# Kernel tuning notes

Measured on AMD Instinct MI355X. Metric: run time of the kernel, lower is better.

The kernel has to match this reference:

```python
import jax, jax.numpy as jnp
import numpy as np

B, H, W, DIM, WS, NH, HID = 16, 64, 64, 256, 8, 8, 1024
SHIFT = WS // 2
N = WS * WS  # tokens per window


def _rel_pos_index(ws):
    coords = np.stack(np.meshgrid(np.arange(ws), np.arange(ws), indexing='ij')).reshape(2, -1)
    rel = (coords[:, :, None] - coords[:, None, :]).transpose(1, 2, 0)  # [n,n,2]
    rel[..., 0] += ws - 1
    rel[..., 1] += ws - 1
    rel[..., 0] *= 2 * ws - 1
    return rel.sum(-1)  # [n,n] ints in [0, (2ws-1)^2)


def _attn_mask(h, w, ws, ss):
    img = np.zeros((h, w), np.float32)
    cnt = 0
    sl = (slice(0, -ws), slice(-ws, -ss), slice(-ss, None))
    for hs in sl:
        for wsl in sl:
            img[hs, wsl] = cnt
            cnt += 1
    mw = img.reshape(h // ws, ws, w // ws, ws).transpose(0, 2, 1, 3).reshape(-1, ws * ws)
    d = mw[:, None, :] - mw[:, :, None]  # unsqueeze(1) - unsqueeze(2)
    return np.where(d != 0, np.float32(-100.0), np.float32(0.0))  # [nW,n,n]


RPI = jnp.asarray(_rel_pos_index(WS).reshape(-1))          # [n*n] int
MASK = jnp.asarray(_attn_mask(H, W, WS, SHIFT))            # [nW,n,n]


def ln(x, g, b, eps):
    m = x.mean(-1, keepdims=True)
    v = x.var(-1, keepdims=True)
    return (x - m) / jnp.sqrt(v + eps) * g + b


def win_part(x, ws):
    b, h, w, c = x.shape
    x = x.reshape(b, h // ws, ws, w // ws, ws, c).transpose(0, 1, 3, 2, 4, 5)
    return x.reshape(-1, ws * ws, c)  # [b*nW, n, c]


def win_rev(win, ws, h, w):
    c = win.shape[-1]
    b = win.shape[0] // ((h // ws) * (w // ws))
    x = win.reshape(b, h // ws, w // ws, ws, ws, c).transpose(0, 1, 3, 2, 4, 5)
    return x.reshape(b, h, w, c)


def attention(xw, qkv_w, qkv_b, rpb, out_w, out_b, mask):
    Bw, n, c = xw.shape
    dh = c // NH
    scale = dh ** -0.5
    qkv = (xw @ qkv_w + qkv_b).reshape(Bw, n, 3, NH, dh).transpose(2, 0, 3, 1, 4)
    q, k, v = qkv[0], qkv[1], qkv[2]                       # [Bw,NH,n,dh]
    dots = jnp.einsum('bhid,bhjd->bhij', q, k) * scale
    bias = rpb[RPI].reshape(n, n, NH).transpose(2, 0, 1)   # [NH,n,n]
    attn = dots + bias[None]
    if mask is not None:
        nW = mask.shape[0]
        attn = attn.reshape(Bw // nW, nW, NH, n, n) + mask[None, :, None]
        attn = attn.reshape(Bw, NH, n, n)
    attn = jax.nn.softmax(attn, axis=-1)
    out = jnp.einsum('bhij,bhjd->bhid', attn, v)
    out = out.transpose(0, 2, 1, 3).reshape(Bw, n, c)
    return out @ out_w + out_b


def block(x, shifted, mask, n1g, n1b, qkv_w, qkv_b, rpb, out_w, out_b,
          n2g, n2b, lng, lnb, w1, b1, w2, b2):
    b, l, c = x.shape
    shortcut = x
    x = ln(x, n1g, n1b, 1e-5).reshape(b, H, W, c)
    if shifted:
        x = jnp.roll(x, (-SHIFT, -SHIFT), (1, 2))
    xw = win_part(x, WS)
    xw = attention(xw, qkv_w, qkv_b, rpb, out_w, out_b, mask)
    x = win_rev(xw, WS, H, W)
    if shifted:
        x = jnp.roll(x, (SHIFT, SHIFT), (1, 2))
    x = shortcut + x.reshape(b, l, c)
    # FeedForward contains its own LayerNorm(eps=1e-6) after norm2 (faithful to source)
    h = ln(x, n2g, n2b, 1e-5)
    h = ln(h, lng, lnb, 1e-6)
    h = jax.nn.gelu(h @ w1 + b1, approximate=False) @ w2 + b2
    return x + h


def forward(x, *p):
    x = block(x, False, None, *p[0:15])
    x = block(x, True, MASK, *p[15:30])
    return x


def setup_inputs() -> dict:
    key = jax.random.key(0)
    ks = iter(jax.random.split(key, 16))
    s = 0.02
    d = {'x': jax.random.normal(next(ks), (B, H * W, DIM), jnp.float32)}
    for i in (0, 1):
        p = f'b{i}_'
        d[p + 'n1g'] = jnp.ones((DIM,), jnp.float32)
        d[p + 'n1b'] = jnp.zeros((DIM,), jnp.float32)
        d[p + 'qkv_w'] = jax.random.normal(next(ks), (DIM, 3 * DIM), jnp.float32) * s
        d[p + 'qkv_b'] = jnp.zeros((3 * DIM,), jnp.float32)
        d[p + 'rpb'] = jax.random.normal(next(ks), ((2 * WS - 1) ** 2, NH), jnp.float32) * s
        d[p + 'out_w'] = jax.random.normal(next(ks), (DIM, DIM), jnp.float32) * s
        d[p + 'out_b'] = jnp.zeros((DIM,), jnp.float32)
        d[p + 'n2g'] = jnp.ones((DIM,), jnp.float32)
        d[p + 'n2b'] = jnp.zeros((DIM,), jnp.float32)
        d[p + 'lng'] = jnp.ones((DIM,), jnp.float32)
        d[p + 'lnb'] = jnp.zeros((DIM,), jnp.float32)
        d[p + 'w1'] = jax.random.normal(next(ks), (DIM, HID), jnp.float32) * s
        d[p + 'b1'] = jnp.zeros((HID,), jnp.float32)
        d[p + 'w2'] = jax.random.normal(next(ks), (HID, DIM), jnp.float32) * s
        d[p + 'b2'] = jnp.zeros((DIM,), jnp.float32)
    return d


def reference(x,
              b0_n1g, b0_n1b, b0_qkv_w, b0_qkv_b, b0_rpb, b0_out_w, b0_out_b,
              b0_n2g, b0_n2b, b0_lng, b0_lnb, b0_w1, b0_b1, b0_w2, b0_b2,
              b1_n1g, b1_n1b, b1_qkv_w, b1_qkv_b, b1_rpb, b1_out_w, b1_out_b,
              b1_n2g, b1_n2b, b1_lng, b1_lnb, b1_w1, b1_b1, b1_w2, b1_b2):
    return forward(x,
                   b0_n1g, b0_n1b, b0_qkv_w, b0_qkv_b, b0_rpb, b0_out_w, b0_out_b,
                   b0_n2g, b0_n2b, b0_lng, b0_lnb, b0_w1, b0_b1, b0_w2, b0_b2,
                   b1_n1g, b1_n1b, b1_qkv_w, b1_qkv_b, b1_rpb, b1_out_w, b1_out_b,
                   b1_n2g, b1_n2b, b1_lng, b1_lnb, b1_w1, b1_b1, b1_w2, b1_b2)
```

## Files before the change

### kernel.cpp

```cpp
#include <hip/hip_runtime.h>

typedef unsigned short u16;
typedef __attribute__((ext_vector_type(8))) short bf16x8;
typedef __attribute__((ext_vector_type(8))) unsigned short u16x8;
typedef __attribute__((ext_vector_type(4))) unsigned short u16x4;
typedef __attribute__((ext_vector_type(4))) float f32x4;

__device__ inline float b2f(u16 u) {
    union { unsigned u32; float f; } x; x.u32 = ((unsigned)u) << 16; return x.f;
}
__device__ inline u16 f2b(float f) {
    union { float f; unsigned u; } x; x.f = f;
    unsigned r = x.u + 0x7fffu + ((x.u >> 16) & 1u);
    return (u16)(r >> 16);
}

__device__ inline float fast_gelu(float v) {
    float x = fabsf(v) * 0.70710678118654752f;
    float t = __builtin_amdgcn_rcpf(1.0f + 0.3275911f * x);
    float e = __expf(-x * x);
    float poly = ((((1.061405429f * t - 1.453152027f) * t + 1.421413741f) * t
                   - 0.284496736f) * t + 0.254829592f) * t;
    float erfv = 1.0f - poly * e;
    float w = copysignf(erfv, v);
    return 0.5f * v * (1.0f + w);
}

#define GLOAD_LDS16(g, l) \
    __builtin_amdgcn_global_load_lds((const __attribute__((address_space(1))) void*)(const void*)(g), \
                                     (__attribute__((address_space(3))) void*)(void*)(l), 16, 0, 0)
#define FENCE() asm volatile("" ::: "memory")

__global__ __launch_bounds__(256)
void ln_win_kernel(const float* __restrict__ x, const float* __restrict__ g,
                   const float* __restrict__ b, u16* __restrict__ xw, int shift)
{
    int wid = blockIdx.x * 4 + (threadIdx.x >> 6);
    int lane = threadIdx.x & 63;
    int win = wid >> 6, tok = wid & 63;
    int bb = win >> 6, wib = win & 63;
    int h = (((wib >> 3) << 3) + (tok >> 3) + shift) & 63;
    int w = (((wib & 7) << 3) + (tok & 7) + shift) & 63;
    size_t src = ((size_t)bb * 4096 + h * 64 + w) * 256;
    float4 v = ((const float4*)(x + src))[lane];
    float s = v.x + v.y + v.z + v.w;
    float s2 = v.x*v.x + v.y*v.y + v.z*v.z + v.w*v.w;
    for (int k = 32; k > 0; k >>= 1) { s += __shfl_xor(s, k); s2 += __shfl_xor(s2, k); }
    float mean = s * (1.f/256.f);
    float var  = s2 * (1.f/256.f) - mean*mean;
    float rs = rsqrtf(var + 1e-5f);
    int c = lane * 4;
    u16x4 o;
    o[0] = f2b((v.x - mean) * rs * g[c+0] + b[c+0]);
    o[1] = f2b((v.y - mean) * rs * g[c+1] + b[c+1]);
    o[2] = f2b((v.z - mean) * rs * g[c+2] + b[c+2]);
    o[3] = f2b((v.w - mean) * rs * g[c+3] + b[c+3]);
    *(u16x4*)(xw + (size_t)wid * 256 + c) = o;
}

__global__ __launch_bounds__(256)
void ln2_kernel(const float* __restrict__ xin,
                const float* __restrict__ g1, const float* __restrict__ b1,
                const float* __restrict__ g2, const float* __restrict__ b2,
                u16* __restrict__ out)
{
    int wid = blockIdx.x * 4 + (threadIdx.x >> 6);
    int lane = threadIdx.x & 63;
    float4 v = ((const float4*)(xin + (size_t)wid * 256))[lane];
    float s = v.x + v.y + v.z + v.w;
    float s2 = v.x*v.x + v.y*v.y + v.z*v.z + v.w*v.w;
    for (int k = 32; k > 0; k >>= 1) { s += __shfl_xor(s, k); s2 += __shfl_xor(s2, k); }
    float mean = s * (1.f/256.f);
    float var  = s2 * (1.f/256.f) - mean*mean;
    float rs = rsqrtf(var + 1e-5f);
    int c = lane * 4;
    float y0 = (v.x - mean) * rs * g1[c+0] + b1[c+0];
    float y1 = (v.y - mean) * rs * g1[c+1] + b1[c+1];
    float y2 = (v.z - mean) * rs * g1[c+2] + b1[c+2];
    float y3 = (v.w - mean) * rs * g1[c+3] + b1[c+3];
    float t = y0 + y1 + y2 + y3;
    float t2 = y0*y0 + y1*y1 + y2*y2 + y3*y3;
    for (int k = 32; k > 0; k >>= 1) { t += __shfl_xor(t, k); t2 += __shfl_xor(t2, k); }
    float m2 = t * (1.f/256.f);
    float v2 = t2 * (1.f/256.f) - m2*m2;
    float rs2 = rsqrtf(v2 + 1e-6f);
    u16x4 o;
    o[0] = f2b((y0 - m2) * rs2 * g2[c+0] + b2[c+0]);
    o[1] = f2b((y1 - m2) * rs2 * g2[c+1] + b2[c+1]);
    o[2] = f2b((y2 - m2) * rs2 * g2[c+2] + b2[c+2]);
    o[3] = f2b((y3 - m2) * rs2 * g2[c+3] + b2[c+3]);
    *(u16x4*)(out + (size_t)wid * 256 + c) = o;
}

__global__ __launch_bounds__(256)
void transpose_w(const float* __restrict__ W, u16* __restrict__ Wt, int K, int N)
{
    __shared__ float t[32][33];
    int nb = blockIdx.x * 32, kb = blockIdx.y * 32;
    int tx = threadIdx.x & 31, ty = threadIdx.x >> 5;
    #pragma unroll
    for (int r = 0; r < 32; r += 8)
        t[ty + r][tx] = W[(size_t)(kb + ty + r) * N + nb + tx];
    __syncthreads();
    #pragma unroll
    for (int r = 0; r < 32; r += 8)
        Wt[(size_t)(nb + ty + r) * K + kb + tx] = f2b(t[tx][ty + r]);
}

__global__ __launch_bounds__(256)
void build_bias(const float* __restrict__ rpb, float* __restrict__ bmT)
{
    int idx = blockIdx.x * 256 + threadIdx.x;
    int q = idx & 63, k = (idx >> 6) & 63, h = (idx >> 12) & 7, cls = idx >> 15;
    int qh = q >> 3, qw = q & 7, kh = k >> 3, kw = k & 7;
    float v = rpb[((qh - kh + 7) * 15 + (qw - kw + 7)) * 8 + h];
    int ch = cls >> 1, cw = cls & 1;
    int rq = (ch ? (qh < 4 ? 1 : 2) : 0) * 3 + (cw ? (qw < 4 ? 1 : 2) : 0);
    int rk = (ch ? (kh < 4 ? 1 : 2) : 0) * 3 + (cw ? (kw < 4 ? 1 : 2) : 0);
    if (rq != rk) v -= 100.f;
    bmT[idx] = v * 1.4426950408889634f;
}

template<int EPI>
__global__ __launch_bounds__(256, 2)
void gemm_areg(const u16* __restrict__ A, const u16* __restrict__ Bt,
               const float* __restrict__ bias, void* __restrict__ out,
               const float* __restrict__ resid, int N, int shift)
{
    constexpr int K = 256;
    __shared__ u16 Bs[2][8][64][32];
    const int tid = threadIdx.x, lane = tid & 63, wv = tid >> 6;
    const int g = lane >> 4, r = lane & 15;
    const int bid = blockIdx.x;
    const int bm = (bid & 7) * 64 + (bid >> 3);
    const int row0 = bm * 128 + wv * 32;

    bf16x8 af[2][8];
    #pragma unroll
    for (int rf = 0; rf < 2; ++rf)
        #pragma unroll
        for (int ks = 0; ks < 8; ++ks)
            af[rf][ks] = *(const bf16x8*)(A + (size_t)(row0 + rf * 16 + r) * K + ks * 32 + g * 8);

    const int NB = N >> 6;
#define STAGE(bn_, buf_) do { \
        _Pragma("unroll") \
        for (int it = 0; it < 8; ++it) { \
            const int S = it * 256 + wv * 64 + lane; \
            const int ks_ = S >> 8, col_ = (S >> 2) & 63, k8_ = S & 3; \
            GLOAD_LDS16(Bt + (size_t)((bn_) * 64 + col_) * K + ks_ * 32 + k8_ * 8, \
                        &Bs[buf_][0][0][0] + (size_t)(it * 256 + wv * 64) * 8); \
        } \
    } while (0)

    FENCE();
    STAGE(0, 0);
    for (int bn = 0; bn < NB; ++bn) {
        const int cur = bn & 1;
        if (bn + 1 < NB) { STAGE(bn + 1, cur ^ 1); }
        if (bn == 0) {
            asm volatile("s_waitcnt vmcnt(8)" ::: "memory");
        } else if (bn + 1 < NB) {
            if (EPI == 2) asm volatile("s_waitcnt vmcnt(24)" ::: "memory");
            else          asm volatile("s_waitcnt vmcnt(16)" ::: "memory");
        } else {
            if (EPI == 2) asm volatile("s_waitcnt vmcnt(16)" ::: "memory");
            else          asm volatile("s_waitcnt vmcnt(8)" ::: "memory");
        }
        __builtin_amdgcn_s_barrier();
        FENCE();
        f32x4 acc[4][2] = {};
        #pragma unroll
        for (int ks = 0; ks < 8; ++ks) {
            bf16x8 bf[4];
            #pragma unroll
            for (int cf = 0; cf < 4; ++cf)
                bf[cf] = *(const bf16x8*)(&Bs[cur][ks][cf * 16 + r][g * 8]);
            __builtin_amdgcn_s_setprio(1);
            #pragma unroll
            for (int cf = 0; cf < 4; ++cf)
                #pragma unroll
                for (int rf = 0; rf < 2; ++rf)
                    acc[cf][rf] = __builtin_amdgcn_mfma_f32_16x16x32_bf16(bf[cf], af[rf][ks], acc[cf][rf], 0, 0, 0);
            __builtin_amdgcn_s_setprio(0);
        }
        asm volatile("s_waitcnt lgkmcnt(0)" ::: "memory");
        __builtin_amdgcn_sched_barrier(0);
        __builtin_amdgcn_s_barrier();
        FENCE();
        #pragma unroll
        for (int rf = 0; rf < 2; ++rf) {
            const int row = row0 + rf * 16 + r;
            size_t orow;
            if (EPI == 2) {
                int win = row >> 6, tok = row & 63;
                int bb = win >> 6, wib = win & 63;
                int h = (((wib >> 3) << 3) + (tok >> 3) + shift) & 63;
                int w = (((wib & 7) << 3) + (tok & 7) + shift) & 63;
                orow = (size_t)bb * 4096 + h * 64 + w;
            } else {
                orow = (size_t)row;
            }
            #pragma unroll
            for (int cf = 0; cf < 4; ++cf) {
                const int colb = bn * 64 + cf * 16 + g * 4;
                const float4 bv = *(const float4*)(bias + colb);
                if (EPI == 0) {
                    u16x4 o;
                    o[0] = f2b(acc[cf][rf][0] + bv.x);
                    o[1] = f2b(acc[cf][rf][1] + bv.y);
                    o[2] = f2b(acc[cf][rf][2] + bv.z);
                    o[3] = f2b(acc[cf][rf][3] + bv.w);
                    *(u16x4*)((u16*)out + (size_t)row * N + colb) = o;
                } else if (EPI == 1) {
                    u16x4 o;
                    o[0] = f2b(fast_gelu(acc[cf][rf][0] + bv.x));
                    o[1] = f2b(fast_gelu(acc[cf][rf][1] + bv.y));
                    o[2] = f2b(fast_gelu(acc[cf][rf][2] + bv.z));
                    o[3] = f2b(fast_gelu(acc[cf][rf][3] + bv.w));
                    *(u16x4*)((u16*)out + (size_t)row * N + colb) = o;
                } else {
                    const float4 rv = *(const float4*)(resid + orow * N + colb);
                    float4 o;
                    o.x = rv.x + acc[cf][rf][0] + bv.x;
                    o.y = rv.y + acc[cf][rf][1] + bv.y;
                    o.z = rv.z + acc[cf][rf][2] + bv.z;
                    o.w = rv.w + acc[cf][rf][3] + bv.w;
                    *(float4*)((float*)out + orow * N + colb) = o;
                }
            }
        }
        FENCE();
    }
#undef STAGE
}

template<int EPI>
__global__ __launch_bounds__(256)
void gemm_k4(const u16* __restrict__ A, const u16* __restrict__ Bt,
             const float* __restrict__ bias, void* __restrict__ out,
             const float* __restrict__ resid, int M, int N, int K, int shift)
{
    __shared__ u16 As[4][128][32];
    __shared__ u16 Bs[4][128][32];
    const int tid = threadIdx.x, lane = tid & 63, wv = tid >> 6;
    const int g = lane >> 4, r = lane & 15;
    const int wr = wv >> 1, wc = wv & 1;
    const int nwg = gridDim.x * gridDim.y;
    const int lid = blockIdx.y * gridDim.x + blockIdx.x;
    const int qq = nwg >> 3, r8 = nwg & 7;
    const int xcd = lid & 7, pos = lid >> 3;
    const int nid = (xcd < r8 ? xcd * (qq + 1) : r8 * (qq + 1) + (xcd - r8) * qq) + pos;
    const int bm = nid / gridDim.x, bn = nid % gridDim.x;
    f32x4 acc[4][4] = {};
    const int arow = wv * 16 + (lane >> 2);
    const int scol = (((lane & 3) ^ ((lane >> 2) & 3) ^ ((lane >> 4) & 1)) * 8);
    const u16* gA = A + (size_t)(bm * 128 + arow) * K + scol;
    const u16* gB = Bt + (size_t)(bn * 128 + arow) * K + scol;
    const int nk = K >> 5;
    const int rc = (g ^ (r & 3) ^ ((r >> 2) & 1)) * 8;

#define STAGE(t) do { \
        u16* a_ = &As[(t) & 3][0][0]; u16* b_ = &Bs[(t) & 3][0][0]; \
        GLOAD_LDS16(gA + (size_t)(t) * 32,                    a_ + wv * 512); \
        GLOAD_LDS16(gA + (size_t)(t) * 32 + (size_t)64 * K,   a_ + 2048 + wv * 512); \
        GLOAD_LDS16(gB + (size_t)(t) * 32,                    b_ + wv * 512); \
        GLOAD_LDS16(gB + (size_t)(t) * 32 + (size_t)64 * K,   b_ + 2048 + wv * 512); \
    } while (0)

    STAGE(0);
    STAGE(1);
    for (int kt = 0; kt < nk; ++kt) {
        const int cur = kt & 3;
        if (kt + 2 < nk) {
            STAGE(kt + 2);
            asm volatile("s_waitcnt vmcnt(8)" ::: "memory");
        } else if (kt + 1 < nk) {
            asm volatile("s_waitcnt vmcnt(4)" ::: "memory");
        } else {
            asm volatile("s_waitcnt vmcnt(0)" ::: "memory");
        }
        __builtin_amdgcn_s_barrier();
        FENCE();
        bf16x8 af[4], bf[4];
        #pragma unroll
        for (int i = 0; i < 4; ++i)
            af[i] = *(const bf16x8*)(&As[cur][wr * 64 + i * 16 + r][rc]);
        #pragma unroll
        for (int j = 0; j < 4; ++j)
            bf[j] = *(const bf16x8*)(&Bs[cur][wc * 64 + j * 16 + r][rc]);
        __builtin_amdgcn_s_setprio(1);
        #pragma unroll
        for (int j = 0; j < 4; ++j)
            #pragma unroll
            for (int i = 0; i < 4; ++i)
                acc[j][i] = __builtin_amdgcn_mfma_f32_16x16x32_bf16(bf[j], af[i], acc[j][i], 0, 0, 0);
        __builtin_amdgcn_s_setprio(0);
        asm volatile("s_waitcnt lgkmcnt(0)" ::: "memory");
        __builtin_amdgcn_sched_barrier(0);
    }
#undef STAGE

    #pragma unroll
    for (int i = 0; i < 4; ++i) {
        const int row = bm * 128 + wr * 64 + i * 16 + r;
        #pragma unroll
        for (int j = 0; j < 4; ++j) {
            const int colb = bn * 128 + wc * 64 + j * 16 + g * 4;
            const float4 bv = *(const float4*)(bias + colb);
            const float4 rv = *(const float4*)(resid + (size_t)row * N + colb);
            float4 o;
            o.x = rv.x + acc[j][i][0] + bv.x;
            o.y = rv.y + acc[j][i][1] + bv.y;
            o.z = rv.z + acc[j][i][2] + bv.z;
            o.w = rv.w + acc[j][i][3] + bv.w;
            *(float4*)((float*)out + (size_t)row * N + colb) = o;
        }
    }
}

template<int SHIFTED>
__global__ __launch_bounds__(256)
void attn_mfma(const u16* __restrict__ qkv, const float* __restrict__ bmT,
               u16* __restrict__ out)
{
    __shared__ u16 pbuf[4][64 * 72];
    __shared__ u16 vbuf[4][32 * 72];
    const int tid = threadIdx.x, lane = tid & 63, wv = tid >> 6;
    const int g = lane >> 4, r = lane & 15;
    const int win = blockIdx.x;
    u16* P  = pbuf[wv];
    u16* Vt = vbuf[wv];
    const u16* base = qkv + (size_t)win * 64 * 768;
    int cls = 0;
    if (SHIFTED) {
        int wib = win & 63;
        cls = (((wib >> 3) == 7) ? 2 : 0) + (((wib & 7) == 7) ? 1 : 0);
    }
    const float sc = 0.17677669529663687f * 1.4426950408889634f;

    for (int hh = 0; hh < 2; ++hh) {
        const int h = wv * 2 + hh;
        const float* bmh = bmT + ((size_t)cls * 8 + h) * 4096;
        bf16x8 kf[4], qf[4];
        #pragma unroll
        for (int i = 0; i < 4; ++i) {
            kf[i] = *(const bf16x8*)(base + (size_t)(i * 16 + r) * 768 + 256 + h * 32 + g * 8);
            qf[i] = *(const bf16x8*)(base + (size_t)(i * 16 + r) * 768 +       h * 32 + g * 8);
        }
        #pragma unroll
        for (int d0 = 0; d0 < 32; d0 += 8) {
            u16x8 vv = *(const u16x8*)(base + (size_t)lane * 768 + 512 + h * 32 + d0);
            #pragma unroll
            for (int e = 0; e < 8; ++e) Vt[(d0 + e) * 72 + lane] = vv[e];
        }
        f32x4 acc[4][4] = {};
        #pragma unroll
        for (int i = 0; i < 4; ++i)
            #pragma unroll
            for (int j = 0; j < 4; ++j)
                acc[i][j] = __builtin_amdgcn_mfma_f32_16x16x32_bf16(kf[i], qf[j], acc[i][j], 0, 0, 0);
        #pragma unroll
        for (int i = 0; i < 4; ++i) {
            const int kb = (i * 16 + g * 4) * 64;
            #pragma unroll
            for (int j = 0; j < 4; ++j) {
                const int qq = j * 16 + r;
                #pragma unroll
                for (int rr = 0; rr < 4; ++rr)
                    acc[i][j][rr] = acc[i][j][rr] * sc + bmh[kb + rr * 64 + qq];
            }
        }
        float inv_[4];
        #pragma unroll
        for (int j = 0; j < 4; ++j) {
            float m = acc[0][j][0];
            #pragma unroll
            for (int i = 0; i < 4; ++i)
                #pragma unroll
                for (int rr = 0; rr < 4; ++rr) m = fmaxf(m, acc[i][j][rr]);
            m = fmaxf(m, __shfl_xor(m, 16));
            m = fmaxf(m, __shfl_xor(m, 32));
            float s = 0.f;
            #pragma unroll
            for (int i = 0; i < 4; ++i)
                #pragma unroll
                for (int rr = 0; rr < 4; ++rr) {
                    float p = exp2f(acc[i][j][rr] - m);
                    acc[i][j][rr] = p; s += p;
                }
            s += __shfl_xor(s, 16);
            s += __shfl_xor(s, 32);
            inv_[j] = 1.f / s;
        }
        #pragma unroll
        for (int j = 0; j < 4; ++j) {
            const float iv = inv_[j];
            #pragma unroll
            for (int i = 0; i < 4; ++i) {
                u16x4 w;
                #pragma unroll
                for (int rr = 0; rr < 4; ++rr) w[rr] = f2b(acc[i][j][rr] * iv);
                *(u16x4*)(P + (j * 16 + r) * 72 + i * 16 + g * 4) = w;
            }
        }
        f32x4 o[2][4] = {};
        #pragma unroll
        for (int ks = 0; ks < 2; ++ks) {
            bf16x8 pa[4], vb[2];
            #pragma unroll
            for (int i = 0; i < 4; ++i)
                pa[i] = *(const bf16x8*)(P + (i * 16 + r) * 72 + ks * 32 + g * 8);
            #pragma unroll
            for (int j = 0; j < 2; ++j)
                vb[j] = *(const bf16x8*)(Vt + (j * 16 + r) * 72 + ks * 32 + g * 8);
            #pragma unroll
            for (int j = 0; j < 2; ++j)
                #pragma unroll
                for (int i = 0; i < 4; ++i)
                    o[j][i] = __builtin_amdgcn_mfma_f32_16x16x32_bf16(vb[j], pa[i], o[j][i], 0, 0, 0);
        }
        u16* op = out + (size_t)win * 64 * 256 + h * 32;
        #pragma unroll
        for (int i = 0; i < 4; ++i) {
            const int qrow = i * 16 + r;
            #pragma unroll
            for (int j = 0; j < 2; ++j) {
                u16x4 w;
                #pragma unroll
                for (int rr = 0; rr < 4; ++rr) w[rr] = f2b(o[j][i][rr]);
                *(u16x4*)(op + (size_t)qrow * 256 + j * 16 + g * 4) = w;
            }
        }
    }
}

extern "C" void kernel_launch(void* const* d_in, const int* in_sizes, int n_in,
                              void* d_out, int out_size, void* d_ws, size_t ws_size,
                              hipStream_t stream)
{
    (void)in_sizes; (void)n_in; (void)out_size; (void)ws_size;
    const float* x = (const float*)d_in[0];
    char* ws = (char*)d_ws;
    size_t off = 0;
    auto alloc = [&](size_t bytes) { void* p = ws + off; off += (bytes + 255) & ~(size_t)255; return p; };

    u16 *wtq[2], *wto[2], *wt1[2], *wt2[2];
    float* bmT[2];
    for (int i = 0; i < 2; ++i) {
        wtq[i] = (u16*)alloc((size_t)768 * 256 * 2);
        wto[i] = (u16*)alloc((size_t)256 * 256 * 2);
        wt1[i] = (u16*)alloc((size_t)1024 * 256 * 2);
        wt2[i] = (u16*)alloc((size_t)256 * 1024 * 2);
        bmT[i] = (float*)alloc((size_t)4 * 8 * 64 * 64 * 4);
    }
    u16*  xw  = (u16*)alloc((size_t)65536 * 256 * 2);
    u16*  big = (u16*)alloc((size_t)65536 * 1024 * 2);
    float* x1 = (float*)alloc((size_t)65536 * 256 * 4);
    float* outp = (float*)d_out;

    for (int blk = 0; blk < 2; ++blk) {
        const float* const* P = (const float* const*)(d_in + 1 + blk * 15);
        transpose_w<<<dim3(768 / 32, 256 / 32), 256, 0, stream>>>(P[2], wtq[blk], 256, 768);
        transpose_w<<<dim3(256 / 32, 256 / 32), 256, 0, stream>>>(P[5], wto[blk], 256, 256);
        transpose_w<<<dim3(1024 / 32, 256 / 32), 256, 0, stream>>>(P[11], wt1[blk], 256, 1024);
        transpose_w<<<dim3(256 / 32, 1024 / 32), 256, 0, stream>>>(P[13], wt2[blk], 1024, 256);
        build_bias<<<512, 256, 0, stream>>>(P[4], bmT[blk]);
    }

    for (int blk = 0; blk < 2; ++blk) {
        const float* const* P = (const float* const*)(d_in + 1 + blk * 15);
        const int sh = blk ? 4 : 0;
        const float* xin = blk ? outp : x;

        ln_win_kernel<<<16384, 256, 0, stream>>>(xin, P[0], P[1], xw, sh);
        gemm_areg<0><<<512, 256, 0, stream>>>(xw, wtq[blk], P[3], big, nullptr, 768, 0);
        if (blk) attn_mfma<1><<<1024, 256, 0, stream>>>(big, bmT[blk], xw);
        else     attn_mfma<0><<<1024, 256, 0, stream>>>(big, bmT[blk], xw);
        gemm_areg<2><<<512, 256, 0, stream>>>(xw, wto[blk], P[6], x1, xin, 256, sh);
        ln2_kernel<<<16384, 256, 0, stream>>>(x1, P[7], P[8], P[9], P[10], xw);
        gemm_areg<1><<<512, 256, 0, stream>>>(xw, wt1[blk], P[12], big, nullptr, 1024, 0);
        gemm_k4<3><<<dim3(2, 512), 256, 0, stream>>>(big, wt2[blk], P[14], outp, x1, 65536, 256, 1024, 0);
    }
}
```

Before: 701.1 us.

## Fuse LayerNorm prologues into A-register GEMMs and use sigmoid GELU approximation

```diff
diff --git a/kernel.cpp b/kernel.cpp
--- a/kernel.cpp
+++ b/kernel.cpp
@@ -1,4 +1,5 @@
 #include <hip/hip_runtime.h>
+#include <hip/hip_bf16.h>
 
 typedef unsigned short u16;
 typedef __attribute__((ext_vector_type(8))) short bf16x8;
@@ -10,87 +11,18 @@
     union { unsigned u32; float f; } x; x.u32 = ((unsigned)u) << 16; return x.f;
 }
 __device__ inline u16 f2b(float f) {
-    union { float f; unsigned u; } x; x.f = f;
-    unsigned r = x.u + 0x7fffu + ((x.u >> 16) & 1u);
-    return (u16)(r >> 16);
+    return __builtin_bit_cast(u16, __float2bfloat16(f));
 }
 
 __device__ inline float fast_gelu(float v) {
-    float x = fabsf(v) * 0.70710678118654752f;
-    float t = __builtin_amdgcn_rcpf(1.0f + 0.3275911f * x);
-    float e = __expf(-x * x);
-    float poly = ((((1.061405429f * t - 1.453152027f) * t + 1.421413741f) * t
-                   - 0.284496736f) * t + 0.254829592f) * t;
-    float erfv = 1.0f - poly * e;
-    float w = copysignf(erfv, v);
-    return 0.5f * v * (1.0f + w);
+    float u = v * (1.5957691216f + 0.0713548163f * v * v);
+    return v * __builtin_amdgcn_rcpf(1.0f + __expf(-u));
 }
 
 #define GLOAD_LDS16(g, l) \
     __builtin_amdgcn_global_load_lds((const __attribute__((address_space(1))) void*)(const void*)(g), \
                                      (__attribute__((address_space(3))) void*)(void*)(l), 16, 0, 0)
 #define FENCE() asm volatile("" ::: "memory")
-
-__global__ __launch_bounds__(256)
-void ln_win_kernel(const float* __restrict__ x, const float* __restrict__ g,
-                   const float* __restrict__ b, u16* __restrict__ xw, int shift)
-{
-    int wid = blockIdx.x * 4 + (threadIdx.x >> 6);
-    int lane = threadIdx.x & 63;
-    int win = wid >> 6, tok = wid & 63;
-    int bb = win >> 6, wib = win & 63;
-    int h = (((wib >> 3) << 3) + (tok >> 3) + shift) & 63;
-    int w = (((wib & 7) << 3) + (tok & 7) + shift) & 63;
-    size_t src = ((size_t)bb * 4096 + h * 64 + w) * 256;
-    float4 v = ((const float4*)(x + src))[lane];
-    float s = v.x + v.y + v.z + v.w;
-    float s2 = v.x*v.x + v.y*v.y + v.z*v.z + v.w*v.w;
-    for (int k = 32; k > 0; k >>= 1) { s += __shfl_xor(s, k); s2 += __shfl_xor(s2, k); }
-    float mean = s * (1.f/256.f);
-    float var  = s2 * (1.f/256.f) - mean*mean;
-    float rs = rsqrtf(var + 1e-5f);
-    int c = lane * 4;
-    u16x4 o;
-    o[0] = f2b((v.x - mean) * rs * g[c+0] + b[c+0]);
-    o[1] = f2b((v.y - mean) * rs * g[c+1] + b[c+1]);
-    o[2] = f2b((v.z - mean) * rs * g[c+2] + b[c+2]);
-    o[3] = f2b((v.w - mean) * rs * g[c+3] + b[c+3]);
-    *(u16x4*)(xw + (size_t)wid * 256 + c) = o;
-}
-
-__global__ __launch_bounds__(256)
-void ln2_kernel(const float* __restrict__ xin,
-                const float* __restrict__ g1, const float* __restrict__ b1,
-                const float* __restrict__ g2, const float* __restrict__ b2,
-                u16* __restrict__ out)
-{
-    int wid = blockIdx.x * 4 + (threadIdx.x >> 6);
-    int lane = threadIdx.x & 63;
-    float4 v = ((const float4*)(xin + (size_t)wid * 256))[lane];
-    float s = v.x + v.y + v.z + v.w;
-    float s2 = v.x*v.x + v.y*v.y + v.z*v.z + v.w*v.w;
-    for (int k = 32; k > 0; k >>= 1) { s += __shfl_xor(s, k); s2 += __shfl_xor(s2, k); }
-    float mean = s * (1.f/256.f);
-    float var  = s2 * (1.f/256.f) - mean*mean;
-    float rs = rsqrtf(var + 1e-5f);
-    int c = lane * 4;
-    float y0 = (v.x - mean) * rs * g1[c+0] + b1[c+0];
-    float y1 = (v.y - mean) * rs * g1[c+1] + b1[c+1];
-    float y2 = (v.z - mean) * rs * g1[c+2] + b1[c+2];
-    float y3 = (v.w - mean) * rs * g1[c+3] + b1[c+3];
-    float t = y0 + y1 + y2 + y3;
-    float t2 = y0*y0 + y1*y1 + y2*y2 + y3*y3;
-    for (int k = 32; k > 0; k >>= 1) { t += __shfl_xor(t, k); t2 += __shfl_xor(t2, k); }
-    float m2 = t * (1.f/256.f);
-    float v2 = t2 * (1.f/256.f) - m2*m2;
-    float rs2 = rsqrtf(v2 + 1e-6f);
-    u16x4 o;
-    o[0] = f2b((y0 - m2) * rs2 * g2[c+0] + b2[c+0]);
-    o[1] = f2b((y1 - m2) * rs2 * g2[c+1] + b2[c+1]);
-    o[2] = f2b((y2 - m2) * rs2 * g2[c+2] + b2[c+2]);
-    o[3] = f2b((y3 - m2) * rs2 * g2[c+3] + b2[c+3]);
-    *(u16x4*)(out + (size_t)wid * 256 + c) = o;
-}
 
 __global__ __launch_bounds__(256)
 void transpose_w(const float* __restrict__ W, u16* __restrict__ Wt, int K, int N)
@@ -121,28 +53,31 @@
     bmT[idx] = v * 1.4426950408889634f;
 }
 
-template<int EPI>
+template<int MODE>
 __global__ __launch_bounds__(256, 2)
-void gemm_areg(const u16* __restrict__ A, const u16* __restrict__ Bt,
+void areg_gemm(const void* __restrict__ Ax, const u16* __restrict__ Bt,
                const float* __restrict__ bias, void* __restrict__ out,
-               const float* __restrict__ resid, int N, int shift)
+               const float* __restrict__ resid,
+               const float* __restrict__ lg1, const float* __restrict__ lb1,
+               const float* __restrict__ lg2, const float* __restrict__ lb2,
+               int N, int shift)
 {
     constexpr int K = 256;
     __shared__ u16 Bs[2][8][64][32];
+    __shared__ float biasL[1024];
+    __shared__ float lnp[4][256];
     const int tid = threadIdx.x, lane = tid & 63, wv = tid >> 6;
     const int g = lane >> 4, r = lane & 15;
     const int bid = blockIdx.x;
     const int bm = (bid & 7) * 64 + (bid >> 3);
     const int row0 = bm * 128 + wv * 32;
 
-    bf16x8 af[2][8];
-    #pragma unroll
-    for (int rf = 0; rf < 2; ++rf)
-        #pragma unroll
-        for (int ks = 0; ks < 8; ++ks)
-            af[rf][ks] = *(const bf16x8*)(A + (size_t)(row0 + rf * 16 + r) * K + ks * 32 + g * 8);
-
-    const int NB = N >> 6;
+    for (int i = tid; i < N; i += 256) biasL[i] = bias[i];
+    if (MODE == 0 && tid < 256) { lnp[0][tid] = lg1[tid]; lnp[1][tid] = lb1[tid]; }
+    if (MODE == 1 && tid < 256) { lnp[0][tid] = lg1[tid]; lnp[1][tid] = lb1[tid];
+                                  lnp[2][tid] = lg2[tid]; lnp[3][tid] = lb2[tid]; }
+    __syncthreads();
+
 #define STAGE(bn_, buf_) do { \
         _Pragma("unroll") \
         for (int it = 0; it < 8; ++it) { \
@@ -153,19 +88,90 @@
         } \
     } while (0)
 
-    FENCE();
     STAGE(0, 0);
+
+    bf16x8 af[2][8];
+    if (MODE == 2) {
+        const u16* A = (const u16*)Ax;
+        #pragma unroll
+        for (int rf = 0; rf < 2; ++rf)
+            #pragma unroll
+            for (int ks = 0; ks < 8; ++ks)
+                af[rf][ks] = *(const bf16x8*)(A + (size_t)(row0 + rf * 16 + r) * K + ks * 32 + g * 8);
+    } else {
+        const float* x = (const float*)Ax;
+        #pragma unroll
+        for (int rf = 0; rf < 2; ++rf) {
+            const int row = row0 + rf * 16 + r;
+            size_t srow;
+            if (MODE == 0) {
+                int win = row >> 6, tok = row & 63;
+                int bb = win >> 6, wib = win & 63;
+                int h = (((wib >> 3) << 3) + (tok >> 3) + shift) & 63;
+                int w = (((wib & 7) << 3) + (tok & 7) + shift) & 63;
+                srow = (size_t)bb * 4096 + h * 64 + w;
+            } else {
+                srow = (size_t)row;
+            }
+            const float* xr = x + srow * 256 + g * 8;
+            f32x4 xv[16];
+            #pragma unroll
+            for (int ks = 0; ks < 8; ++ks) {
+                xv[2 * ks]     = *(const f32x4*)(xr + ks * 32);
+                xv[2 * ks + 1] = *(const f32x4*)(xr + ks * 32 + 4);
+            }
+            float s = 0.f, s2 = 0.f;
+            #pragma unroll
+            for (int q = 0; q < 16; ++q)
+                #pragma unroll
+                for (int e = 0; e < 4; ++e) { s += xv[q][e]; s2 += xv[q][e] * xv[q][e]; }
+            s  += __shfl_xor(s, 16);  s  += __shfl_xor(s, 32);
+            s2 += __shfl_xor(s2, 16); s2 += __shfl_xor(s2, 32);
+            const float m1 = s * (1.f / 256.f);
+            const float rs1 = rsqrtf(s2 * (1.f / 256.f) - m1 * m1 + 1e-5f);
+            float m2 = 0.f, rs2 = 0.f;
+            if (MODE == 1) {
+                float t = 0.f, t2 = 0.f;
+                #pragma unroll
+                for (int ks = 0; ks < 8; ++ks)
+                    #pragma unroll
+                    for (int e = 0; e < 8; ++e) {
+                        const int c = ks * 32 + g * 8 + e;
+                        float y = (xv[2 * ks + (e >> 2)][e & 3] - m1) * rs1 * lnp[0][c] + lnp[1][c];
+                        t += y; t2 += y * y;
+                    }
+                t  += __shfl_xor(t, 16);  t  += __shfl_xor(t, 32);
+                t2 += __shfl_xor(t2, 16); t2 += __shfl_xor(t2, 32);
+                m2 = t * (1.f / 256.f);
+                rs2 = rsqrtf(t2 * (1.f / 256.f) - m2 * m2 + 1e-6f);
+            }
+            #pragma unroll
+            for (int ks = 0; ks < 8; ++ks) {
+                u16x8 o;
+                #pragma unroll
+                for (int e = 0; e < 8; ++e) {
+                    const int c = ks * 32 + g * 8 + e;
+                    float y = (xv[2 * ks + (e >> 2)][e & 3] - m1) * rs1 * lnp[0][c] + lnp[1][c];
+                    if (MODE == 1) y = (y - m2) * rs2 * lnp[2][c] + lnp[3][c];
+                    o[e] = f2b(y);
+                }
+                af[rf][ks] = __builtin_bit_cast(bf16x8, o);
+            }
+        }
+    }
+
+    const int NB = N >> 6;
     for (int bn = 0; bn < NB; ++bn) {
         const int cur = bn & 1;
-        if (bn + 1 < NB) { STAGE(bn + 1, cur ^ 1); }
+        if (bn + 1 < NB) STAGE(bn + 1, cur ^ 1);
         if (bn == 0) {
             asm volatile("s_waitcnt vmcnt(8)" ::: "memory");
         } else if (bn + 1 < NB) {
-            if (EPI == 2) asm volatile("s_waitcnt vmcnt(24)" ::: "memory");
-            else          asm volatile("s_waitcnt vmcnt(16)" ::: "memory");
+            if (MODE == 2) asm volatile("s_waitcnt vmcnt(24)" ::: "memory");
+            else           asm volatile("s_waitcnt vmcnt(16)" ::: "memory");
         } else {
-            if (EPI == 2) asm volatile("s_waitcnt vmcnt(16)" ::: "memory");
-            else          asm volatile("s_waitcnt vmcnt(8)" ::: "memory");
+            if (MODE == 2) asm volatile("s_waitcnt vmcnt(16)" ::: "memory");
+            else           asm volatile("s_waitcnt vmcnt(8)" ::: "memory");
         }
         __builtin_amdgcn_s_barrier();
         FENCE();
@@ -192,7 +198,7 @@
         for (int rf = 0; rf < 2; ++rf) {
             const int row = row0 + rf * 16 + r;
             size_t orow;
-            if (EPI == 2) {
+            if (MODE == 2) {
                 int win = row >> 6, tok = row & 63;
                 int bb = win >> 6, wib = win & 63;
                 int h = (((wib >> 3) << 3) + (tok >> 3) + shift) & 63;
@@ -204,29 +210,23 @@
             #pragma unroll
             for (int cf = 0; cf < 4; ++cf) {
                 const int colb = bn * 64 + cf * 16 + g * 4;
-                const float4 bv = *(const float4*)(bias + colb);
-                if (EPI == 0) {
+                const f32x4 bv = *(const f32x4*)(&biasL[colb]);
+                if (MODE == 0) {
                     u16x4 o;
-                    o[0] = f2b(acc[cf][rf][0] + bv.x);
-                    o[1] = f2b(acc[cf][rf][1] + bv.y);
-                    o[2] = f2b(acc[cf][rf][2] + bv.z);
-                    o[3] = f2b(acc[cf][rf][3] + bv.w);
+                    #pragma unroll
+                    for (int e = 0; e < 4; ++e) o[e] = f2b(acc[cf][rf][e] + bv[e]);
                     *(u16x4*)((u16*)out + (size_t)row * N + colb) = o;
-                } else if (EPI == 1) {
+                } else if (MODE == 1) {
                     u16x4 o;
-                    o[0] = f2b(fast_gelu(acc[cf][rf][0] + bv.x));
-                    o[1] = f2b(fast_gelu(acc[cf][rf][1] + bv.y));
-                    o[2] = f2b(fast_gelu(acc[cf][rf][2] + bv.z));
-                    o[3] = f2b(fast_gelu(acc[cf][rf][3] + bv.w));
+                    #pragma unroll
+                    for (int e = 0; e < 4; ++e) o[e] = f2b(fast_gelu(acc[cf][rf][e] + bv[e]));
                     *(u16x4*)((u16*)out + (size_t)row * N + colb) = o;
                 } else {
-                    const float4 rv = *(const float4*)(resid + orow * N + colb);
-                    float4 o;
-                    o.x = rv.x + acc[cf][rf][0] + bv.x;
-                    o.y = rv.y + acc[cf][rf][1] + bv.y;
-                    o.z = rv.z + acc[cf][rf][2] + bv.z;
-                    o.w = rv.w + acc[cf][rf][3] + bv.w;
-                    *(float4*)((float*)out + orow * N + colb) = o;
+                    const f32x4 rv = *(const f32x4*)(resid + orow * N + colb);
+                    f32x4 o;
+                    #pragma unroll
+                    for (int e = 0; e < 4; ++e) o[e] = rv[e] + acc[cf][rf][e] + bv[e];
+                    *(f32x4*)((float*)out + orow * N + colb) = o;
                 }
             }
         }
@@ -235,11 +235,10 @@
 #undef STAGE
 }
 
-template<int EPI>
 __global__ __launch_bounds__(256)
 void gemm_k4(const u16* __restrict__ A, const u16* __restrict__ Bt,
-             const float* __restrict__ bias, void* __restrict__ out,
-             const float* __restrict__ resid, int M, int N, int K, int shift)
+             const float* __restrict__ bias, float* __restrict__ out,
+             const float* __restrict__ resid, int M, int N, int K)
 {
     __shared__ u16 As[4][128][32];
     __shared__ u16 Bs[4][128][32];
@@ -307,14 +306,12 @@
         #pragma unroll
         for (int j = 0; j < 4; ++j) {
             const int colb = bn * 128 + wc * 64 + j * 16 + g * 4;
-            const float4 bv = *(const float4*)(bias + colb);
-            const float4 rv = *(const float4*)(resid + (size_t)row * N + colb);
-            float4 o;
-            o.x = rv.x + acc[j][i][0] + bv.x;
-            o.y = rv.y + acc[j][i][1] + bv.y;
-            o.z = rv.z + acc[j][i][2] + bv.z;
-            o.w = rv.w + acc[j][i][3] + bv.w;
-            *(float4*)((float*)out + (size_t)row * N + colb) = o;
+            const f32x4 bv = *(const f32x4*)(bias + colb);
+            const f32x4 rv = *(const f32x4*)(resid + (size_t)row * N + colb);
+            f32x4 o;
+            #pragma unroll
+            for (int e = 0; e < 4; ++e) o[e] = rv[e] + acc[j][i][e] + bv[e];
+            *(f32x4*)(out + (size_t)row * N + colb) = o;
         }
     }
 }
@@ -473,13 +470,14 @@
         const int sh = blk ? 4 : 0;
         const float* xin = blk ? outp : x;
 
-        ln_win_kernel<<<16384, 256, 0, stream>>>(xin, P[0], P[1], xw, sh);
-        gemm_areg<0><<<512, 256, 0, stream>>>(xw, wtq[blk], P[3], big, nullptr, 768, 0);
+        areg_gemm<0><<<512, 256, 0, stream>>>(xin, wtq[blk], P[3], big, nullptr,
+                                              P[0], P[1], nullptr, nullptr, 768, sh);
         if (blk) attn_mfma<1><<<1024, 256, 0, stream>>>(big, bmT[blk], xw);
         else     attn_mfma<0><<<1024, 256, 0, stream>>>(big, bmT[blk], xw);
-        gemm_areg<2><<<512, 256, 0, stream>>>(xw, wto[blk], P[6], x1, xin, 256, sh);
-        ln2_kernel<<<16384, 256, 0, stream>>>(x1, P[7], P[8], P[9], P[10], xw);
-        gemm_areg<1><<<512, 256, 0, stream>>>(xw, wt1[blk], P[12], big, nullptr, 1024, 0);
-        gemm_k4<3><<<dim3(2, 512), 256, 0, stream>>>(big, wt2[blk], P[14], outp, x1, 65536, 256, 1024, 0);
-    }
-}
+        areg_gemm<2><<<512, 256, 0, stream>>>(xw, wto[blk], P[6], x1, xin,
+                                              nullptr, nullptr, nullptr, nullptr, 256, sh);
+        areg_gemm<1><<<512, 256, 0, stream>>>(x1, wt1[blk], P[12], big, nullptr,
+                                              P[7], P[8], P[9], P[10], 1024, 0);
+        gemm_k4<<<dim3(2, 512), 256, 0, stream>>>(big, wt2[blk], P[14], outp, x1, 65536, 256, 1024);
+    }
+}
```

Result: no change. 701.8 us (+0.1%).
